# Kernel tuning notes

Hardware: AMD Instinct MI355X
Metric: run time of the kernel (lower is better)

Reference implementation:

```python
import jax, jax.numpy as jnp
import numpy as np

B, N = 4096, 2048


def setup_inputs() -> dict:
    key = jax.random.key(0)
    k1, k2, k3, k4 = jax.random.split(key, 4)
    return {
        "src_pts3d": jax.random.normal(k1, (B, N, 3), dtype=jnp.float32),
        "tgt_pts3d": jax.random.normal(k2, (B, N, 3), dtype=jnp.float32),
        "kpt_src_mask": jax.random.uniform(k3, (B, N), dtype=jnp.float32),
        "kpt_tgt_mask": jax.random.uniform(k4, (B, N), dtype=jnp.float32),
    }


def reference(src_pts3d, tgt_pts3d, kpt_src_mask, kpt_tgt_mask):
    # H = src^T @ diag(mask_tgt) @ tgt, fused as a masked row-scale contraction: [B,3,3]
    H = jnp.einsum('bnc,bn,bnd->bcd', src_pts3d, kpt_tgt_mask, tgt_pts3d)
    # torch.svd returns V (H = U S V^T); jnp returns Vh, so V = Vh^T
    u, s, vh = jnp.linalg.svd(H)
    v = jnp.swapaxes(vh, -1, -2)              # [B,3,3]
    ut = jnp.swapaxes(u, -1, -2)              # [B,3,3]
    r = v @ ut
    det = jnp.linalg.det(r)                   # [B]
    # branch-free reflection fix: negate 3rd column of V when det(r) < 0
    sign = jnp.where(det < 0, -1.0, 1.0)
    col_scale = jnp.stack([jnp.ones_like(sign), jnp.ones_like(sign), sign], axis=-1)  # [B,3]
    R = (v * col_scale[:, None, :]) @ ut
    return R
```

## Files before the change

### kernel.cpp

```cpp
#include <hip/hip_runtime.h>
#include <math.h>

#define BATCH 4096
#define NPTS  2048
#define THREADS 256

typedef float f32x4 __attribute__((ext_vector_type(4)));

__device__ __forceinline__ f32x4 ntload(const f32x4* p) {
    return __builtin_nontemporal_load(p);
}

#define ACC(sx, sy, sz, tx, ty, tz, mm) do {                                   \
    float d0 = (mm) * (tx), d1 = (mm) * (ty), d2 = (mm) * (tz);                \
    h[0] = fmaf((sx), d0, h[0]); h[1] = fmaf((sx), d1, h[1]); h[2] = fmaf((sx), d2, h[2]); \
    h[3] = fmaf((sy), d0, h[3]); h[4] = fmaf((sy), d1, h[4]); h[5] = fmaf((sy), d2, h[5]); \
    h[6] = fmaf((sz), d0, h[6]); h[7] = fmaf((sz), d1, h[7]); h[8] = fmaf((sz), d2, h[8]); \
} while (0)

__global__ __launch_bounds__(THREADS, 4)
void fused_kernel(const float* __restrict__ src, const float* __restrict__ tgt,
                  const float* __restrict__ mask, float* __restrict__ out)
{
    const int b   = blockIdx.x;
    const int t   = threadIdx.x;
    const f32x4* s4 = (const f32x4*)(src  + (size_t)b * (NPTS * 3));
    const f32x4* t4 = (const f32x4*)(tgt  + (size_t)b * (NPTS * 3));
    const f32x4* m4 = (const f32x4*)(mask + (size_t)b * NPTS);

    f32x4 m0  = ntload(&m4[t]);
    f32x4 m1  = ntload(&m4[t + 256]);
    f32x4 sa0 = ntload(&s4[3 * t + 0]);
    f32x4 sb0 = ntload(&s4[3 * t + 1]);
    f32x4 sc0 = ntload(&s4[3 * t + 2]);
    f32x4 ta0 = ntload(&t4[3 * t + 0]);
    f32x4 tb0 = ntload(&t4[3 * t + 1]);
    f32x4 tc0 = ntload(&t4[3 * t + 2]);
    f32x4 sa1 = ntload(&s4[3 * (t + 256) + 0]);
    f32x4 sb1 = ntload(&s4[3 * (t + 256) + 1]);
    f32x4 sc1 = ntload(&s4[3 * (t + 256) + 2]);
    f32x4 ta1 = ntload(&t4[3 * (t + 256) + 0]);
    f32x4 tb1 = ntload(&t4[3 * (t + 256) + 1]);
    f32x4 tc1 = ntload(&t4[3 * (t + 256) + 2]);

    float h[9] = {0.f, 0.f, 0.f, 0.f, 0.f, 0.f, 0.f, 0.f, 0.f};
    ACC(sa0.x, sa0.y, sa0.z, ta0.x, ta0.y, ta0.z, m0.x);
    ACC(sa0.w, sb0.x, sb0.y, ta0.w, tb0.x, tb0.y, m0.y);
    ACC(sb0.z, sb0.w, sc0.x, tb0.z, tb0.w, tc0.x, m0.z);
    ACC(sc0.y, sc0.z, sc0.w, tc0.y, tc0.z, tc0.w, m0.w);
    ACC(sa1.x, sa1.y, sa1.z, ta1.x, ta1.y, ta1.z, m1.x);
    ACC(sa1.w, sb1.x, sb1.y, ta1.w, tb1.x, tb1.y, m1.y);
    ACC(sb1.z, sb1.w, sc1.x, tb1.z, tb1.w, tc1.x, m1.z);
    ACC(sc1.y, sc1.z, sc1.w, tc1.y, tc1.z, tc1.w, m1.w);

#pragma unroll
    for (int off = 32; off > 0; off >>= 1) {
#pragma unroll
        for (int i = 0; i < 9; ++i) h[i] += __shfl_down(h[i], off);
    }

    __shared__ float shred[THREADS / 64][9];
    const int wid  = t >> 6;
    const int lane = t & 63;
    if (lane == 0) {
#pragma unroll
        for (int i = 0; i < 9; ++i) shred[wid][i] = h[i];
    }
    __syncthreads();

    if (t != 0) return;

    double H[3][3];
#pragma unroll
    for (int i = 0; i < 9; ++i)
        H[i / 3][i % 3] = (double)(shred[0][i] + shred[1][i] +
                                   shred[2][i] + shred[3][i]);

    double A[3][3];
#pragma unroll
    for (int i = 0; i < 3; ++i)
#pragma unroll
        for (int j = 0; j < 3; ++j)
            A[i][j] = H[0][i] * H[0][j] + H[1][i] * H[1][j] + H[2][i] * H[2][j];

    double V[3][3] = {{1, 0, 0}, {0, 1, 0}, {0, 0, 1}};

    for (int sweep = 0; sweep < 6; ++sweep) {
#pragma unroll
        for (int r = 0; r < 3; ++r) {
            const int p = (r == 2) ? 1 : 0;
            const int q = (r == 0) ? 1 : 2;
            const int k = (r == 0) ? 2 : ((r == 1) ? 1 : 0);
            double apq = A[p][q];
            if (fabs(apq) > 1e-300) {
                double theta = (A[q][q] - A[p][p]) / (2.0 * apq);
                double tt = 1.0 / (fabs(theta) + sqrt(theta * theta + 1.0));
                if (theta < 0.0) tt = -tt;
                double c = 1.0 / sqrt(tt * tt + 1.0);
                double s = tt * c;
                double app = A[p][p], aqq = A[q][q];
                A[p][p] = app - tt * apq;
                A[q][q] = aqq + tt * apq;
                A[p][q] = A[q][p] = 0.0;
                double akp = A[k][p], akq = A[k][q];
                A[k][p] = A[p][k] = c * akp - s * akq;
                A[k][q] = A[q][k] = s * akp + c * akq;
#pragma unroll
                for (int i = 0; i < 3; ++i) {
                    double vip = V[i][p], viq = V[i][q];
                    V[i][p] = c * vip - s * viq;
                    V[i][q] = s * vip + c * viq;
                }
            }
        }
    }

    const double d0 = A[0][0], d1 = A[1][1], d2 = A[2][2];
    const bool g01 = (d0 >= d1);
    const bool g02 = (d0 >= d2);
    const bool g12 = (d1 >= d2);
    const bool l0 = g01 && g02;
    const bool l1 = (!g01) && g12;

    double v0[3], v1[3];
#pragma unroll
    for (int i = 0; i < 3; ++i) {
        const double c0 = V[i][0], c1 = V[i][1], c2 = V[i][2];
        v0[i] = l0 ? c0 : (l1 ? c1 : c2);
        const double s_l0 = g12 ? c1 : c2;
        const double s_l1 = g02 ? c0 : c2;
        const double s_l2 = g01 ? c0 : c1;
        v1[i] = l0 ? s_l0 : (l1 ? s_l1 : s_l2);
    }

    double b0[3], b1[3];
#pragma unroll
    for (int r = 0; r < 3; ++r) {
        b0[r] = H[r][0] * v0[0] + H[r][1] * v0[1] + H[r][2] * v0[2];
        b1[r] = H[r][0] * v1[0] + H[r][1] * v1[1] + H[r][2] * v1[2];
    }
    double n0 = b0[0] * b0[0] + b0[1] * b0[1] + b0[2] * b0[2];
    double inv0 = 1.0 / sqrt(fmax(n0, 1e-300));
    double u0[3] = {b0[0] * inv0, b0[1] * inv0, b0[2] * inv0};
    double d01 = u0[0] * b1[0] + u0[1] * b1[1] + u0[2] * b1[2];
    double w[3] = {b1[0] - d01 * u0[0], b1[1] - d01 * u0[1], b1[2] - d01 * u0[2]};
    double nw = w[0] * w[0] + w[1] * w[1] + w[2] * w[2];
    double inv1 = 1.0 / sqrt(fmax(nw, 1e-300));
    double u1[3] = {w[0] * inv1, w[1] * inv1, w[2] * inv1};
    double u2[3] = {u0[1] * u1[2] - u0[2] * u1[1],
                    u0[2] * u1[0] - u0[0] * u1[2],
                    u0[0] * u1[1] - u0[1] * u1[0]};
    double vc2[3] = {v0[1] * v1[2] - v0[2] * v1[1],
                     v0[2] * v1[0] - v0[0] * v1[2],
                     v0[0] * v1[1] - v0[1] * v1[0]};

    float* o = out + (size_t)b * 9;
#pragma unroll
    for (int r = 0; r < 3; ++r)
#pragma unroll
        for (int c = 0; c < 3; ++c)
            o[r * 3 + c] = (float)(v0[r] * u0[c] + v1[r] * u1[c] + vc2[r] * u2[c]);
}

extern "C" void kernel_launch(void* const* d_in, const int* in_sizes, int n_in,
                              void* d_out, int out_size, void* d_ws, size_t ws_size,
                              hipStream_t stream) {
    const float* src  = (const float*)d_in[0];
    const float* tgt  = (const float*)d_in[1];
    const float* mask = (const float*)d_in[3];
    float* out = (float*)d_out;

    fused_kernel<<<BATCH, THREADS, 0, stream>>>(src, tgt, mask, out);
}
```

Measured before the change: 246.9 us.

## Process four batches per block with software-pipelined prefetch of next batch

Each block now handles four consecutive batch items, prefetching the first half of the next item's points while accumulating the current one, and uses double-buffered shared memory for the cross-wave reduction. The per-item SVD solve is moved into a noinline device function run by thread 0. The aim is to hide the serial double-precision Jacobi solve and the memory latency behind loads for the next item, and to cut block launch overhead. The cost is that the whole block now waits at each __syncthreads while thread 0 runs the previous item's solve, and the extra prefetch registers add pressure at the same launch bounds.

```diff
diff --git a/kernel.cpp b/kernel.cpp
--- a/kernel.cpp
+++ b/kernel.cpp
@@ -4,6 +4,8 @@
 #define BATCH 4096
 #define NPTS  2048
 #define THREADS 256
+#define BPB 4
+#define GRID (BATCH / BPB)
 
 typedef float f32x4 __attribute__((ext_vector_type(4)));
 
@@ -18,63 +20,36 @@
     h[6] = fmaf((sz), d0, h[6]); h[7] = fmaf((sz), d1, h[7]); h[8] = fmaf((sz), d2, h[8]); \
 } while (0)
 
-__global__ __launch_bounds__(THREADS, 4)
-void fused_kernel(const float* __restrict__ src, const float* __restrict__ tgt,
-                  const float* __restrict__ mask, float* __restrict__ out)
+#define DECL_HALF(P) f32x4 P##m, P##sa, P##sb, P##sc, P##ta, P##tb, P##tc;
+
+#define LOAD_HALF(P, bb, g) do {                                               \
+    const f32x4* s4_ = (const f32x4*)(src  + (size_t)(bb) * (NPTS * 3));       \
+    const f32x4* t4_ = (const f32x4*)(tgt  + (size_t)(bb) * (NPTS * 3));       \
+    const f32x4* m4_ = (const f32x4*)(mask + (size_t)(bb) * NPTS);             \
+    const int g_ = (g);                                                        \
+    P##m  = ntload(&m4_[g_]);                                                  \
+    P##sa = ntload(&s4_[3 * g_ + 0]);                                          \
+    P##sb = ntload(&s4_[3 * g_ + 1]);                                          \
+    P##sc = ntload(&s4_[3 * g_ + 2]);                                          \
+    P##ta = ntload(&t4_[3 * g_ + 0]);                                          \
+    P##tb = ntload(&t4_[3 * g_ + 1]);                                          \
+    P##tc = ntload(&t4_[3 * g_ + 2]);                                          \
+} while (0)
+
+#define FMA_HALF(P) do {                                                       \
+    ACC(P##sa.x, P##sa.y, P##sa.z, P##ta.x, P##ta.y, P##ta.z, P##m.x);         \
+    ACC(P##sa.w, P##sb.x, P##sb.y, P##ta.w, P##tb.x, P##tb.y, P##m.y);         \
+    ACC(P##sb.z, P##sb.w, P##sc.x, P##tb.z, P##tb.w, P##tc.x, P##m.z);         \
+    ACC(P##sc.y, P##sc.z, P##sc.w, P##tc.y, P##tc.z, P##tc.w, P##m.w);         \
+} while (0)
+
+__device__ __attribute__((noinline))
+void solve_one(float f0, float f1, float f2, float f3, float f4, float f5,
+               float f6, float f7, float f8, float* __restrict__ o)
 {
-    const int b   = blockIdx.x;
-    const int t   = threadIdx.x;
-    const f32x4* s4 = (const f32x4*)(src  + (size_t)b * (NPTS * 3));
-    const f32x4* t4 = (const f32x4*)(tgt  + (size_t)b * (NPTS * 3));
-    const f32x4* m4 = (const f32x4*)(mask + (size_t)b * NPTS);
-
-    f32x4 m0  = ntload(&m4[t]);
-    f32x4 m1  = ntload(&m4[t + 256]);
-    f32x4 sa0 = ntload(&s4[3 * t + 0]);
-    f32x4 sb0 = ntload(&s4[3 * t + 1]);
-    f32x4 sc0 = ntload(&s4[3 * t + 2]);
-    f32x4 ta0 = ntload(&t4[3 * t + 0]);
-    f32x4 tb0 = ntload(&t4[3 * t + 1]);
-    f32x4 tc0 = ntload(&t4[3 * t + 2]);
-    f32x4 sa1 = ntload(&s4[3 * (t + 256) + 0]);
-    f32x4 sb1 = ntload(&s4[3 * (t + 256) + 1]);
-    f32x4 sc1 = ntload(&s4[3 * (t + 256) + 2]);
-    f32x4 ta1 = ntload(&t4[3 * (t + 256) + 0]);
-    f32x4 tb1 = ntload(&t4[3 * (t + 256) + 1]);
-    f32x4 tc1 = ntload(&t4[3 * (t + 256) + 2]);
-
-    float h[9] = {0.f, 0.f, 0.f, 0.f, 0.f, 0.f, 0.f, 0.f, 0.f};
-    ACC(sa0.x, sa0.y, sa0.z, ta0.x, ta0.y, ta0.z, m0.x);
-    ACC(sa0.w, sb0.x, sb0.y, ta0.w, tb0.x, tb0.y, m0.y);
-    ACC(sb0.z, sb0.w, sc0.x, tb0.z, tb0.w, tc0.x, m0.z);
-    ACC(sc0.y, sc0.z, sc0.w, tc0.y, tc0.z, tc0.w, m0.w);
-    ACC(sa1.x, sa1.y, sa1.z, ta1.x, ta1.y, ta1.z, m1.x);
-    ACC(sa1.w, sb1.x, sb1.y, ta1.w, tb1.x, tb1.y, m1.y);
-    ACC(sb1.z, sb1.w, sc1.x, tb1.z, tb1.w, tc1.x, m1.z);
-    ACC(sc1.y, sc1.z, sc1.w, tc1.y, tc1.z, tc1.w, m1.w);
-
-#pragma unroll
-    for (int off = 32; off > 0; off >>= 1) {
-#pragma unroll
-        for (int i = 0; i < 9; ++i) h[i] += __shfl_down(h[i], off);
-    }
-
-    __shared__ float shred[THREADS / 64][9];
-    const int wid  = t >> 6;
-    const int lane = t & 63;
-    if (lane == 0) {
-#pragma unroll
-        for (int i = 0; i < 9; ++i) shred[wid][i] = h[i];
-    }
-    __syncthreads();
-
-    if (t != 0) return;
-
-    double H[3][3];
-#pragma unroll
-    for (int i = 0; i < 9; ++i)
-        H[i / 3][i % 3] = (double)(shred[0][i] + shred[1][i] +
-                                   shred[2][i] + shred[3][i]);
+    double H[3][3] = {{(double)f0, (double)f1, (double)f2},
+                      {(double)f3, (double)f4, (double)f5},
+                      {(double)f6, (double)f7, (double)f8}};
 
     double A[3][3];
 #pragma unroll
@@ -154,12 +129,61 @@
                      v0[2] * v1[0] - v0[0] * v1[2],
                      v0[0] * v1[1] - v0[1] * v1[0]};
 
-    float* o = out + (size_t)b * 9;
 #pragma unroll
     for (int r = 0; r < 3; ++r)
 #pragma unroll
         for (int c = 0; c < 3; ++c)
             o[r * 3 + c] = (float)(v0[r] * u0[c] + v1[r] * u1[c] + vc2[r] * u2[c]);
+}
+
+__global__ __launch_bounds__(THREADS, 4)
+void fused_kernel(const float* __restrict__ src, const float* __restrict__ tgt,
+                  const float* __restrict__ mask, float* __restrict__ out)
+{
+    const int t    = threadIdx.x;
+    const int b0   = blockIdx.x * BPB;
+    const int wid  = t >> 6;
+    const int lane = t & 63;
+
+    __shared__ float shred[2][THREADS / 64][9];
+
+    DECL_HALF(A0) DECL_HALF(A1) DECL_HALF(B_)
+
+#define HS(jj, i) (shred[(jj) & 1][0][i] + shred[(jj) & 1][1][i] + \
+                   shred[(jj) & 1][2][i] + shred[(jj) & 1][3][i])
+
+#define ITER(CUR, NXT, jj, DO_PREF) do {                                       \
+    LOAD_HALF(B_, b0 + (jj), t + 256);                                         \
+    float h[9] = {0.f, 0.f, 0.f, 0.f, 0.f, 0.f, 0.f, 0.f, 0.f};               \
+    FMA_HALF(CUR);                                                             \
+    if (DO_PREF) { LOAD_HALF(NXT, b0 + (jj) + 1, t); }                         \
+    FMA_HALF(B_);                                                              \
+    _Pragma("unroll")                                                          \
+    for (int off = 32; off > 0; off >>= 1) {                                   \
+        _Pragma("unroll")                                                      \
+        for (int i = 0; i < 9; ++i) h[i] += __shfl_down(h[i], off);            \
+    }                                                                          \
+    if (lane == 0) {                                                           \
+        _Pragma("unroll")                                                      \
+        for (int i = 0; i < 9; ++i) shred[(jj) & 1][wid][i] = h[i];            \
+    }                                                                          \
+    __syncthreads();                                                           \
+    if (t == 0) {                                                              \
+        solve_one(HS(jj, 0), HS(jj, 1), HS(jj, 2),                             \
+                  HS(jj, 3), HS(jj, 4), HS(jj, 5),                             \
+                  HS(jj, 6), HS(jj, 7), HS(jj, 8),                             \
+                  out + (size_t)(b0 + (jj)) * 9);                              \
+    }                                                                          \
+} while (0)
+
+    LOAD_HALF(A0, b0, t);
+    ITER(A0, A1, 0, 1);
+    ITER(A1, A0, 1, 1);
+    ITER(A0, A1, 2, 1);
+    ITER(A1, A0, 3, 0);
+
+#undef ITER
+#undef HS
 }
 
 extern "C" void kernel_launch(void* const* d_in, const int* in_sizes, int n_in,
@@ -170,5 +194,5 @@
     const float* mask = (const float*)d_in[3];
     float* out = (float*)d_out;
 
-    fused_kernel<<<BATCH, THREADS, 0, stream>>>(src, tgt, mask, out);
+    fused_kernel<<<GRID, THREADS, 0, stream>>>(src, tgt, mask, out);
 }
```

Result: slower. 252.0 us (+2.1%).
